# Kernel optimization log

Measured on AMD Instinct MI355X. Metric: run time of the kernel, lower is better.

Reference implementation:

```python
import jax, jax.numpy as jnp
import numpy as np

B, N, H = 4, 256, 128
T = 8  # triplet hidden width


def _linear_init(key, fan_in, fan_out):
    s = 1.0 / np.sqrt(fan_in)
    kw, kb = jax.random.split(key)
    W = jax.random.uniform(kw, (fan_in, fan_out), minval=-s, maxval=s, dtype=jnp.float32)
    b = jax.random.uniform(kb, (fan_out,), minval=-s, maxval=s, dtype=jnp.float32)
    return W, b


def setup_inputs() -> dict:
    key = jax.random.key(0)
    ks = jax.random.split(key, 16)
    inp = {
        "node_embeddings": jax.random.normal(ks[0], (B, N, H), dtype=jnp.float32),
        "edge_embeddings": jax.random.normal(ks[1], (B, N, H), dtype=jnp.float32),
        "graph_embeddings": jax.random.normal(ks[2], (B, H), dtype=jnp.float32),
        "previous_hidden": jax.random.normal(ks[3], (B, N, H), dtype=jnp.float32),
    }
    # message MLP: (z_i 2H, z_j 2H, edge_j H, graph H) = 6H -> H -> H -> H
    inp["Wm1"], inp["bm1"] = _linear_init(ks[4], 6 * H, H)
    inp["Wm2"], inp["bm2"] = _linear_init(ks[5], H, H)
    inp["Wm3"], inp["bm3"] = _linear_init(ks[6], H, H)
    # gate MLP: (z 2H, m H, edge H, graph H) = 5H -> H -> H (sigmoid)
    inp["Wg1"], inp["bg1"] = _linear_init(ks[7], 5 * H, H)
    inp["Wg2"], inp["bg2"] = _linear_init(ks[8], H, H)
    # readout: (z 2H, m H) = 3H -> H
    inp["Wr"], inp["br"] = _linear_init(ks[9], 3 * H, H)
    # triplet MLP: (node_j H, node_k H, node H, edge 3H, graph H) = 7H -> 8 (relu)
    inp["Wt1"], inp["bt1"] = _linear_init(ks[10], 7 * H, T)
    # triplet edge readout: 8 -> H
    inp["Wt2"], inp["bt2"] = _linear_init(ks[11], T, H)
    # layer norm params
    inp["gamma"] = jnp.ones((H,), dtype=jnp.float32)
    inp["beta"] = jnp.zeros((H,), dtype=jnp.float32)
    return inp


def reference(node_embeddings, edge_embeddings, graph_embeddings, previous_hidden,
              Wm1, bm1, Wm2, bm2, Wm3, bm3,
              Wg1, bg1, Wg2, bg2, Wr, br,
              Wt1, bt1, Wt2, bt2, gamma, beta):
    h = node_embeddings.shape[-1]
    z = jnp.concatenate([node_embeddings, previous_hidden], axis=-1)  # [B,N,2H]

    # ---- pairwise messages: decompose first linear so the 6H-wide concat is never built ----
    W_zi, W_zj = Wm1[: 2 * h], Wm1[2 * h: 4 * h]
    W_e, W_g = Wm1[4 * h: 5 * h], Wm1[5 * h:]
    u = z @ W_zi + (graph_embeddings @ W_g)[:, None, :] + bm1   # per-i part [B,N,H]
    v = z @ W_zj + edge_embeddings @ W_e                        # per-j part [B,N,H]
    h1 = jax.nn.relu(u[:, :, None, :] + v[:, None, :, :])       # [B,Ni,Nj,H]
    h2 = jax.nn.relu(h1 @ Wm2 + bm2)
    msgs = h2 @ Wm3 + bm3                                       # [B,Ni,Nj,H]
    m = jnp.max(msgs, axis=2)                                   # max over j -> [B,N,H]

    gb = jnp.broadcast_to(graph_embeddings[:, None, :], node_embeddings.shape)
    gate_in = jnp.concatenate([z, m, edge_embeddings, gb], axis=-1)  # [B,N,5H]
    g = jax.nn.sigmoid(jax.nn.relu(gate_in @ Wg1 + bg1) @ Wg2 + bg2)
    h_i = jnp.concatenate([z, m], axis=-1) @ Wr + br
    h_g = g * h_i + (1.0 - g) * previous_hidden

    # ---- triplet messages ----
    # pre-activation is separable over (j, k, i), so max over the N^2 (k,j) pairs
    # equals per-channel max_j + max_k (relu is monotone, max commutes with it).
    Wt_j, Wt_k, Wt_n = Wt1[:h], Wt1[h: 2 * h], Wt1[2 * h: 3 * h]
    Wt_e = Wt1[3 * h: 4 * h] + Wt1[4 * h: 5 * h] + Wt1[5 * h: 6 * h]
    Wt_g = Wt1[6 * h:]
    a_j = node_embeddings @ Wt_j   # [B,N,8]
    a_k = node_embeddings @ Wt_k   # [B,N,8]
    c = node_embeddings @ Wt_n + edge_embeddings @ Wt_e + (graph_embeddings @ Wt_g)[:, None, :] + bt1
    t_max = jax.nn.relu(c + jnp.max(a_j, axis=1, keepdims=True) + jnp.max(a_k, axis=1, keepdims=True))
    h_ij = t_max @ Wt2 + bt2       # [B,N,H]

    # ---- layer norm on gated hidden ----
    mu = jnp.mean(h_g, axis=-1, keepdims=True)
    var = jnp.mean(jnp.square(h_g - mu), axis=-1, keepdims=True)
    h_norm = (h_g - mu) * jax.lax.rsqrt(var + 1e-5) * gamma + beta
    return (h_norm, h_ij)
```

## Files before the change

### kernel.cpp

```cpp
#include <hip/hip_runtime.h>
#include <hip/hip_bf16.h>

typedef unsigned short u16;
typedef unsigned int u32;
typedef float f32x4 __attribute__((ext_vector_type(4)));
typedef short s16x8 __attribute__((ext_vector_type(8)));

#define MFMA16(a,b,c) __builtin_amdgcn_mfma_f32_16x16x32_bf16((a),(b),(c),0,0,0)

static __device__ __forceinline__ u16 f2bf(float x){
  union { __hip_bfloat16 b; u16 u; } c;
  c.b = __float2bfloat16(x);
  return c.u;
}

__global__ void prep_kernel(const float* __restrict__ Wm1, const float* __restrict__ Wm2,
                            const float* __restrict__ Wm3, const float* __restrict__ Wg1,
                            const float* __restrict__ Wr,  const float* __restrict__ Wt1,
                            const float* __restrict__ node,const float* __restrict__ prev,
                            const float* __restrict__ edge,const float* __restrict__ graph,
                            u16* __restrict__ WbT, u16* __restrict__ WgrT,
                            u16* __restrict__ Wm2T, u16* __restrict__ Wm3T,
                            u16* __restrict__ gin)
{
  int idx = blockIdx.x * 256 + threadIdx.x;
  if (idx < 147456) {
    int n = idx >> 9, k = idx & 511;
    int part = k >> 7, kk = k & 127;
    float v = 0.f;
    if (n < 128) {
      if (part == 0)      v = Wm1[kk*128 + n];
      else if (part == 1) v = Wm1[(128+kk)*128 + n];
      else if (part == 3) v = Wm1[(640+kk)*128 + n];
    } else if (n < 256) {
      int nn = n - 128;
      if (part == 0)      v = Wm1[(256+kk)*128 + nn];
      else if (part == 1) v = Wm1[(384+kk)*128 + nn];
      else if (part == 2) v = Wm1[(512+kk)*128 + nn];
    } else if (n < 280) {
      int tt = n - 256;
      if (tt < 8)       { if (part == 0) v = Wt1[kk*8 + tt]; }
      else if (tt < 16) { if (part == 0) v = Wt1[(128+kk)*8 + (tt-8)]; }
      else {
        int t = tt - 16;
        if (part == 0)      v = Wt1[(256+kk)*8 + t];
        else if (part == 2) v = Wt1[(384+kk)*8 + t] + Wt1[(512+kk)*8 + t] + Wt1[(640+kk)*8 + t];
        else if (part == 3) v = Wt1[(768+kk)*8 + t];
      }
    }
    WbT[idx] = f2bf(v);
    return;
  }
  idx -= 147456;
  if (idx < 163840) {
    int n = idx / 640, k = idx - n*640;
    int part = k >> 7, kk = k & 127;
    float v = 0.f;
    if (n < 128) {
      int r = (part==0) ? kk : (part==1) ? (128+kk) : (part==2) ? (384+kk)
                        : (part==3) ? (512+kk) : (256+kk);
      v = Wg1[r*128 + n];
    } else {
      int nn = n - 128;
      if (part == 0)      v = Wr[kk*128 + nn];
      else if (part == 1) v = Wr[(128+kk)*128 + nn];
      else if (part == 4) v = Wr[(256+kk)*128 + nn];
    }
    WgrT[idx] = f2bf(v);
    return;
  }
  idx -= 163840;
  if (idx < 16384) { int n = idx >> 7, k = idx & 127; Wm2T[idx] = f2bf(Wm2[k*128 + n]); return; }
  idx -= 16384;
  if (idx < 16384) { int n = idx >> 7, k = idx & 127; Wm3T[idx] = f2bf(Wm3[k*128 + n]); return; }
  idx -= 16384;
  {
    int row = idx >> 9, k = idx & 511;
    int part = k >> 7, kk = k & 127;
    float v;
    if (part == 0)      v = node[row*128 + kk];
    else if (part == 1) v = prev[row*128 + kk];
    else if (part == 2) v = edge[row*128 + kk];
    else                v = graph[(row >> 8)*128 + kk];
    gin[row*640 + k] = f2bf(v);
  }
}

__global__ void gemm_uvt_kernel(const u16* __restrict__ gin, const u16* __restrict__ WbT,
                                float* __restrict__ uvt)
{
  int m0 = blockIdx.x * 16, n0 = blockIdx.y * 16;
  int lane = threadIdx.x;
  int lrow = lane & 15, lgrp = lane >> 4;
  const u16* arow = gin + (size_t)(m0 + lrow) * 640;
  const u16* brow = WbT + (size_t)(n0 + lrow) * 512;
  f32x4 acc = {0.f, 0.f, 0.f, 0.f};
#pragma unroll
  for (int k0 = 0; k0 < 16; ++k0) {
    s16x8 a = *reinterpret_cast<const s16x8*>(arow + k0*32 + lgrp*8);
    s16x8 b = *reinterpret_cast<const s16x8*>(brow + k0*32 + lgrp*8);
    acc = MFMA16(a, b, acc);
  }
#pragma unroll
  for (int r = 0; r < 4; ++r)
    uvt[(size_t)(m0 + lgrp*4 + r) * 288 + n0 + lrow] = acc[r];
}

__global__ void maxat_kernel(const float* __restrict__ uvt, float* __restrict__ mjk)
{
  int b = blockIdx.x;
  int tid = threadIdx.x;
  int row = b*256 + tid;
  __shared__ float part[4][16];
  float v[16];
#pragma unroll
  for (int t = 0; t < 16; ++t) v[t] = uvt[(size_t)row*288 + 256 + t];
#pragma unroll
  for (int off = 32; off >= 1; off >>= 1) {
#pragma unroll
    for (int t = 0; t < 16; ++t) v[t] = fmaxf(v[t], __shfl_xor(v[t], off));
  }
  int wid = tid >> 6;
  if ((tid & 63) == 0) {
#pragma unroll
    for (int t = 0; t < 16; ++t) part[wid][t] = v[t];
  }
  __syncthreads();
  if (tid < 16)
    mjk[b*16 + tid] = fmaxf(fmaxf(part[0][tid], part[1][tid]),
                            fmaxf(part[2][tid], part[3][tid]));
}

__global__ __launch_bounds__(256) void msgmax_kernel(const float* __restrict__ uvt,
    const u16* __restrict__ Wm2T, const u16* __restrict__ Wm3T,
    const float* __restrict__ bm1, const float* __restrict__ bm2,
    const float* __restrict__ bm3, u16* __restrict__ gin)
{
  const int row = blockIdx.x;
  const int b   = row >> 8;
  const int tid = threadIdx.x;
  const int w   = tid >> 6;
  const int lane = tid & 63;
  const int c = lane & 15, g = lane >> 4;

  __shared__ u16 a1s[2][4][16][32];
  __shared__ u16 h2s[2][16][136];

  s16x8 wb2[4][2], wb3[4][2];
#pragma unroll
  for (int mt = 0; mt < 2; ++mt) {
    int col = w*32 + mt*16 + c;
#pragma unroll
    for (int k0 = 0; k0 < 4; ++k0) {
      wb2[k0][mt] = *reinterpret_cast<const s16x8*>(Wm2T + col*128 + k0*32 + g*8);
      wb3[k0][mt] = *reinterpret_cast<const s16x8*>(Wm3T + col*128 + k0*32 + g*8);
    }
  }
  float4 bm2v[2];
#pragma unroll
  for (int mt = 0; mt < 2; ++mt)
    bm2v[mt] = *reinterpret_cast<const float4*>(bm2 + w*32 + mt*16 + 4*g);

  const float* urow = uvt + (size_t)row * 288;
  float uf[8];
  {
    int off = w*32 + g*8;
    float4 x = *reinterpret_cast<const float4*>(urow + off);
    float4 y = *reinterpret_cast<const float4*>(urow + off + 4);
    float4 p = *reinterpret_cast<const float4*>(bm1 + off);
    float4 q = *reinterpret_cast<const float4*>(bm1 + off + 4);
    uf[0]=x.x+p.x; uf[1]=x.y+p.y; uf[2]=x.z+p.z; uf[3]=x.w+p.w;
    uf[4]=y.x+q.x; uf[5]=y.y+q.y; uf[6]=y.z+q.z; uf[7]=y.w+q.w;
  }

  const float* vb = uvt + (size_t)(b*256) * 288 + 128;
  f32x4 mmax[2];
#pragma unroll
  for (int mt = 0; mt < 2; ++mt)
#pragma unroll
    for (int r = 0; r < 4; ++r) mmax[mt][r] = -1e30f;

  float4 vc[2][2];
#define LOADV(IT) do { \
  _Pragma("unroll") \
  for (int t = 0; t < 2; ++t) { \
    const float* p_ = vb + (size_t)((IT)*32 + t*16 + c) * 288 + w*32 + g*8; \
    vc[t][0] = *reinterpret_cast<const float4*>(p_); \
    vc[t][1] = *reinterpret_cast<const float4*>(p_ + 4); } } while (0)

  LOADV(0);

  for (int it = 0; it < 8; ++it) {
#pragma unroll
    for (int t = 0; t < 2; ++t) {
      u32 d0 = (u32)f2bf(fmaxf(uf[0] + vc[t][0].x, 0.f))
             | ((u32)f2bf(fmaxf(uf[1] + vc[t][0].y, 0.f)) << 16);
      u32 d1 = (u32)f2bf(fmaxf(uf[2] + vc[t][0].z, 0.f))
             | ((u32)f2bf(fmaxf(uf[3] + vc[t][0].w, 0.f)) << 16);
      u32 d2 = (u32)f2bf(fmaxf(uf[4] + vc[t][1].x, 0.f))
             | ((u32)f2bf(fmaxf(uf[5] + vc[t][1].y, 0.f)) << 16);
      u32 d3 = (u32)f2bf(fmaxf(uf[6] + vc[t][1].z, 0.f))
             | ((u32)f2bf(fmaxf(uf[7] + vc[t][1].w, 0.f)) << 16);
      uint4 pk = {d0, d1, d2, d3};
      *reinterpret_cast<uint4*>(&a1s[t][w][c][g*8]) = pk;
    }
    if (it < 7) LOADV(it + 1);
    __syncthreads();

    f32x4 acc1[2][2] = {{{0,0,0,0},{0,0,0,0}},{{0,0,0,0},{0,0,0,0}}};
#pragma unroll
    for (int t = 0; t < 2; ++t)
#pragma unroll
      for (int k0 = 0; k0 < 4; ++k0) {
        s16x8 af = *reinterpret_cast<const s16x8*>(&a1s[t][k0][c][g*8]);
        acc1[t][0] = MFMA16(wb2[k0][0], af, acc1[t][0]);
        acc1[t][1] = MFMA16(wb2[k0][1], af, acc1[t][1]);
      }

#pragma unroll
    for (int t = 0; t < 2; ++t)
#pragma unroll
      for (int mt = 0; mt < 2; ++mt) {
        u32 lo = (u32)f2bf(fmaxf(acc1[t][mt][0] + bm2v[mt].x, 0.f))
               | ((u32)f2bf(fmaxf(acc1[t][mt][1] + bm2v[mt].y, 0.f)) << 16);
        u32 hi = (u32)f2bf(fmaxf(acc1[t][mt][2] + bm2v[mt].z, 0.f))
               | ((u32)f2bf(fmaxf(acc1[t][mt][3] + bm2v[mt].w, 0.f)) << 16);
        uint2 pk = {lo, hi};
        *reinterpret_cast<uint2*>(&h2s[t][c][w*32 + mt*16 + 4*g]) = pk;
      }
    __syncthreads();

    f32x4 acc2[2][2] = {{{0,0,0,0},{0,0,0,0}},{{0,0,0,0},{0,0,0,0}}};
#pragma unroll
    for (int t = 0; t < 2; ++t)
#pragma unroll
      for (int k0 = 0; k0 < 4; ++k0) {
        s16x8 a2 = *reinterpret_cast<const s16x8*>(&h2s[t][c][k0*32 + g*8]);
        acc2[t][0] = MFMA16(wb3[k0][0], a2, acc2[t][0]);
        acc2[t][1] = MFMA16(wb3[k0][1], a2, acc2[t][1]);
      }
#pragma unroll
    for (int mt = 0; mt < 2; ++mt)
#pragma unroll
      for (int r = 0; r < 4; ++r)
        mmax[mt][r] = fmaxf(mmax[mt][r], fmaxf(acc2[0][mt][r], acc2[1][mt][r]));
  }
#undef LOADV

#pragma unroll
  for (int mt = 0; mt < 2; ++mt) {
    f32x4 m = mmax[mt];
#pragma unroll
    for (int off = 1; off < 16; off <<= 1) {
      m[0] = fmaxf(m[0], __shfl_xor(m[0], off));
      m[1] = fmaxf(m[1], __shfl_xor(m[1], off));
      m[2] = fmaxf(m[2], __shfl_xor(m[2], off));
      m[3] = fmaxf(m[3], __shfl_xor(m[3], off));
    }
    if (c == 0) {
      int col = w*32 + mt*16 + 4*g;
      u32 lo = (u32)f2bf(m[0] + bm3[col])   | ((u32)f2bf(m[1] + bm3[col+1]) << 16);
      u32 hi = (u32)f2bf(m[2] + bm3[col+2]) | ((u32)f2bf(m[3] + bm3[col+3]) << 16);
      uint2 pk = {lo, hi};
      *reinterpret_cast<uint2*>(gin + (size_t)row*640 + 512 + col) = pk;
    }
  }
}

__global__ void gemm_gate_kernel(const u16* __restrict__ gin, const u16* __restrict__ WgrT,
                                 const float* __restrict__ bg1, const float* __restrict__ br,
                                 float* __restrict__ r1, float* __restrict__ hi)
{
  int m0 = blockIdx.x * 16, n0 = blockIdx.y * 16;
  int lane = threadIdx.x;
  int lrow = lane & 15, lgrp = lane >> 4;
  const u16* arow = gin  + (size_t)(m0 + lrow) * 640;
  const u16* brow = WgrT + (size_t)(n0 + lrow) * 640;
  f32x4 acc = {0.f, 0.f, 0.f, 0.f};
#pragma unroll
  for (int k0 = 0; k0 < 20; ++k0) {
    s16x8 a = *reinterpret_cast<const s16x8*>(arow + k0*32 + lgrp*8);
    s16x8 b = *reinterpret_cast<const s16x8*>(brow + k0*32 + lgrp*8);
    acc = MFMA16(a, b, acc);
  }
  int col = n0 + lrow;
  float bv = (col < 128) ? bg1[col] : br[col - 128];
#pragma unroll
  for (int r = 0; r < 4; ++r) {
    int gr = m0 + lgrp*4 + r;
    if (col < 128) r1[gr*128 + col] = fmaxf(acc[r] + bv, 0.f);
    else           hi[gr*128 + col - 128] = acc[r] + bv;
  }
}

__global__ void finalize_kernel(const float* __restrict__ r1, const float* __restrict__ hi,
                                const float* __restrict__ prev, const float* __restrict__ uvt,
                                const float* __restrict__ mjk,
                                const float* __restrict__ Wg2, const float* __restrict__ bg2,
                                const float* __restrict__ bt1, const float* __restrict__ Wt2,
                                const float* __restrict__ bt2, const float* __restrict__ gamma,
                                const float* __restrict__ beta, float* __restrict__ out)
{
  int row = blockIdx.x;
  int h = threadIdx.x;
  int b = row >> 8;
  __shared__ float r1s[128];
  __shared__ float red[4];
  r1s[h] = r1[row*128 + h];
  __syncthreads();
  float glin = bg2[h];
#pragma unroll 8
  for (int k = 0; k < 128; ++k) glin += r1s[k] * Wg2[k*128 + h];
  float g = 1.f / (1.f + __expf(-glin));
  float hg = g * hi[row*128 + h] + (1.f - g) * prev[row*128 + h];

  float s1 = hg, s2 = hg*hg;
#pragma unroll
  for (int off = 1; off < 64; off <<= 1) {
    s1 += __shfl_xor(s1, off);
    s2 += __shfl_xor(s2, off);
  }
  int wid = h >> 6;
  if ((h & 63) == 0) { red[wid] = s1; red[2 + wid] = s2; }
  __syncthreads();
  float mu  = (red[0] + red[1]) * 0.0078125f;
  float ex2 = (red[2] + red[3]) * 0.0078125f;
  float var = ex2 - mu*mu;
  float hn = (hg - mu) * rsqrtf(var + 1e-5f) * gamma[h] + beta[h];
  out[row*128 + h] = hn;

  float o2 = bt2[h];
#pragma unroll
  for (int t = 0; t < 8; ++t) {
    float tv = uvt[(size_t)row*288 + 272 + t] + bt1[t] + mjk[b*16 + t] + mjk[b*16 + 8 + t];
    tv = fmaxf(tv, 0.f);
    o2 += tv * Wt2[t*128 + h];
  }
  out[131072 + row*128 + h] = o2;
}

extern "C" void kernel_launch(void* const* d_in, const int* in_sizes, int n_in,
                              void* d_out, int out_size, void* d_ws, size_t ws_size,
                              hipStream_t stream) {
  const float* node  = (const float*)d_in[0];
  const float* edge  = (const float*)d_in[1];
  const float* graph = (const float*)d_in[2];
  const float* prev  = (const float*)d_in[3];
  const float* Wm1 = (const float*)d_in[4];
  const float* bm1 = (const float*)d_in[5];
  const float* Wm2 = (const float*)d_in[6];
  const float* bm2 = (const float*)d_in[7];
  const float* Wm3 = (const float*)d_in[8];
  const float* bm3 = (const float*)d_in[9];
  const float* Wg1 = (const float*)d_in[10];
  const float* bg1 = (const float*)d_in[11];
  const float* Wg2 = (const float*)d_in[12];
  const float* bg2 = (const float*)d_in[13];
  const float* Wr  = (const float*)d_in[14];
  const float* br  = (const float*)d_in[15];
  const float* Wt1 = (const float*)d_in[16];
  const float* bt1 = (const float*)d_in[17];
  const float* Wt2 = (const float*)d_in[18];
  const float* bt2 = (const float*)d_in[19];
  const float* gamma = (const float*)d_in[20];
  const float* beta  = (const float*)d_in[21];
  float* out = (float*)d_out;

  char* ws = (char*)d_ws;
  u16*   WbT  = (u16*)(ws + 0);
  u16*   WgrT = (u16*)(ws + 294912);
  u16*   Wm2T = (u16*)(ws + 622592);
  u16*   Wm3T = (u16*)(ws + 655360);
  u16*   gin  = (u16*)(ws + 688128);
  float* uvt  = (float*)(ws + 1998848);
  float* r1   = (float*)(ws + 3178496);
  float* hi   = (float*)(ws + 3702784);
  float* mjk  = (float*)(ws + 4227072);

  prep_kernel<<<3392, 256, 0, stream>>>(Wm1, Wm2, Wm3, Wg1, Wr, Wt1,
                                        node, prev, edge, graph,
                                        WbT, WgrT, Wm2T, Wm3T, gin);
  gemm_uvt_kernel<<<dim3(64, 18), 64, 0, stream>>>(gin, WbT, uvt);
  maxat_kernel<<<4, 256, 0, stream>>>(uvt, mjk);
  msgmax_kernel<<<1024, 256, 0, stream>>>(uvt, Wm2T, Wm3T, bm1, bm2, bm3, gin);
  gemm_gate_kernel<<<dim3(64, 16), 64, 0, stream>>>(gin, WgrT, bg1, br, r1, hi);
  finalize_kernel<<<1024, 128, 0, stream>>>(r1, hi, prev, uvt, mjk,
                                            Wg2, bg2, bt1, Wt2, bt2, gamma, beta, out);
}
```

Before: 61.21 us.

## Software-pipeline msgmax GEMM stages with double-buffered LDS and fewer barriers

Restructures the msgmax inner loop so that GEMM2 of the current tile and GEMM1 of the next tile share one barrier interval, with a1s and h2s double-buffered and global loads prefetched two iterations ahead. This halves the __syncthreads per iteration and lets MFMA work of adjacent stages interleave. It also pads the a1s rows from 32 to 40 elements to reduce LDS bank conflicts, and adds a min-blocks hint of 4 to the launch bounds. The cost is more LDS, more live registers for the deeper prefetch, and occupancy pressure from the launch-bounds hint.

```diff
diff --git a/kernel.cpp b/kernel.cpp
--- a/kernel.cpp
+++ b/kernel.cpp
@@ -131,7 +131,7 @@
                             fmaxf(part[2][tid], part[3][tid]));
 }
 
-__global__ __launch_bounds__(256) void msgmax_kernel(const float* __restrict__ uvt,
+__global__ __launch_bounds__(256, 4) void msgmax_kernel(const float* __restrict__ uvt,
     const u16* __restrict__ Wm2T, const u16* __restrict__ Wm3T,
     const float* __restrict__ bm1, const float* __restrict__ bm2,
     const float* __restrict__ bm3, u16* __restrict__ gin)
@@ -143,8 +143,8 @@
   const int lane = tid & 63;
   const int c = lane & 15, g = lane >> 4;
 
-  __shared__ u16 a1s[2][4][16][32];
-  __shared__ u16 h2s[2][16][136];
+  __shared__ u16 a1s[2][2][4][16][40];
+  __shared__ u16 h2s[2][2][16][136];
 
   s16x8 wb2[4][2], wb3[4][2];
 #pragma unroll
@@ -188,64 +188,77 @@
     vc[t][0] = *reinterpret_cast<const float4*>(p_); \
     vc[t][1] = *reinterpret_cast<const float4*>(p_ + 4); } } while (0)
 
+#define A1W(BUF) do { \
+  _Pragma("unroll") \
+  for (int t = 0; t < 2; ++t) { \
+    u32 d0 = (u32)f2bf(fmaxf(uf[0] + vc[t][0].x, 0.f)) \
+           | ((u32)f2bf(fmaxf(uf[1] + vc[t][0].y, 0.f)) << 16); \
+    u32 d1 = (u32)f2bf(fmaxf(uf[2] + vc[t][0].z, 0.f)) \
+           | ((u32)f2bf(fmaxf(uf[3] + vc[t][0].w, 0.f)) << 16); \
+    u32 d2 = (u32)f2bf(fmaxf(uf[4] + vc[t][1].x, 0.f)) \
+           | ((u32)f2bf(fmaxf(uf[5] + vc[t][1].y, 0.f)) << 16); \
+    u32 d3 = (u32)f2bf(fmaxf(uf[6] + vc[t][1].z, 0.f)) \
+           | ((u32)f2bf(fmaxf(uf[7] + vc[t][1].w, 0.f)) << 16); \
+    uint4 pk = {d0, d1, d2, d3}; \
+    *reinterpret_cast<uint4*>(&a1s[BUF][t][w][c][g*8]) = pk; } } while (0)
+
+#define GEMM1(AB, HB) do { \
+  f32x4 acc1[2][2] = {{{0,0,0,0},{0,0,0,0}},{{0,0,0,0},{0,0,0,0}}}; \
+  _Pragma("unroll") \
+  for (int t = 0; t < 2; ++t) \
+    _Pragma("unroll") \
+    for (int k0 = 0; k0 < 4; ++k0) { \
+      s16x8 af = *reinterpret_cast<const s16x8*>(&a1s[AB][t][k0][c][g*8]); \
+      acc1[t][0] = MFMA16(wb2[k0][0], af, acc1[t][0]); \
+      acc1[t][1] = MFMA16(wb2[k0][1], af, acc1[t][1]); \
+    } \
+  _Pragma("unroll") \
+  for (int t = 0; t < 2; ++t) \
+    _Pragma("unroll") \
+    for (int mt = 0; mt < 2; ++mt) { \
+      u32 lo = (u32)f2bf(fmaxf(acc1[t][mt][0] + bm2v[mt].x, 0.f)) \
+             | ((u32)f2bf(fmaxf(acc1[t][mt][1] + bm2v[mt].y, 0.f)) << 16); \
+      u32 hi = (u32)f2bf(fmaxf(acc1[t][mt][2] + bm2v[mt].z, 0.f)) \
+             | ((u32)f2bf(fmaxf(acc1[t][mt][3] + bm2v[mt].w, 0.f)) << 16); \
+      uint2 pk = {lo, hi}; \
+      *reinterpret_cast<uint2*>(&h2s[HB][t][c][w*32 + mt*16 + 4*g]) = pk; } } while (0)
+
+#define GEMM2(HB) do { \
+  f32x4 acc2[2][2] = {{{0,0,0,0},{0,0,0,0}},{{0,0,0,0},{0,0,0,0}}}; \
+  _Pragma("unroll") \
+  for (int t = 0; t < 2; ++t) \
+    _Pragma("unroll") \
+    for (int k0 = 0; k0 < 4; ++k0) { \
+      s16x8 a2 = *reinterpret_cast<const s16x8*>(&h2s[HB][t][c][k0*32 + g*8]); \
+      acc2[t][0] = MFMA16(wb3[k0][0], a2, acc2[t][0]); \
+      acc2[t][1] = MFMA16(wb3[k0][1], a2, acc2[t][1]); \
+    } \
+  _Pragma("unroll") \
+  for (int mt = 0; mt < 2; ++mt) \
+    _Pragma("unroll") \
+    for (int r = 0; r < 4; ++r) \
+      mmax[mt][r] = fmaxf(mmax[mt][r], fmaxf(acc2[0][mt][r], acc2[1][mt][r])); } while (0)
+
   LOADV(0);
+  A1W(0);
+  LOADV(1);
+  __syncthreads();
+  GEMM1(0, 0);
 
   for (int it = 0; it < 8; ++it) {
-#pragma unroll
-    for (int t = 0; t < 2; ++t) {
-      u32 d0 = (u32)f2bf(fmaxf(uf[0] + vc[t][0].x, 0.f))
-             | ((u32)f2bf(fmaxf(uf[1] + vc[t][0].y, 0.f)) << 16);
-      u32 d1 = (u32)f2bf(fmaxf(uf[2] + vc[t][0].z, 0.f))
-             | ((u32)f2bf(fmaxf(uf[3] + vc[t][0].w, 0.f)) << 16);
-      u32 d2 = (u32)f2bf(fmaxf(uf[4] + vc[t][1].x, 0.f))
-             | ((u32)f2bf(fmaxf(uf[5] + vc[t][1].y, 0.f)) << 16);
-      u32 d3 = (u32)f2bf(fmaxf(uf[6] + vc[t][1].z, 0.f))
-             | ((u32)f2bf(fmaxf(uf[7] + vc[t][1].w, 0.f)) << 16);
-      uint4 pk = {d0, d1, d2, d3};
-      *reinterpret_cast<uint4*>(&a1s[t][w][c][g*8]) = pk;
-    }
-    if (it < 7) LOADV(it + 1);
+    int nb = (it + 1) & 1;
+    if (it < 7) {
+      A1W(nb);
+      if (it < 6) LOADV(it + 2);
+    }
     __syncthreads();
-
-    f32x4 acc1[2][2] = {{{0,0,0,0},{0,0,0,0}},{{0,0,0,0},{0,0,0,0}}};
-#pragma unroll
-    for (int t = 0; t < 2; ++t)
-#pragma unroll
-      for (int k0 = 0; k0 < 4; ++k0) {
-        s16x8 af = *reinterpret_cast<const s16x8*>(&a1s[t][k0][c][g*8]);
-        acc1[t][0] = MFMA16(wb2[k0][0], af, acc1[t][0]);
-        acc1[t][1] = MFMA16(wb2[k0][1], af, acc1[t][1]);
-      }
-
-#pragma unroll
-    for (int t = 0; t < 2; ++t)
-#pragma unroll
-      for (int mt = 0; mt < 2; ++mt) {
-        u32 lo = (u32)f2bf(fmaxf(acc1[t][mt][0] + bm2v[mt].x, 0.f))
-               | ((u32)f2bf(fmaxf(acc1[t][mt][1] + bm2v[mt].y, 0.f)) << 16);
-        u32 hi = (u32)f2bf(fmaxf(acc1[t][mt][2] + bm2v[mt].z, 0.f))
-               | ((u32)f2bf(fmaxf(acc1[t][mt][3] + bm2v[mt].w, 0.f)) << 16);
-        uint2 pk = {lo, hi};
-        *reinterpret_cast<uint2*>(&h2s[t][c][w*32 + mt*16 + 4*g]) = pk;
-      }
-    __syncthreads();
-
-    f32x4 acc2[2][2] = {{{0,0,0,0},{0,0,0,0}},{{0,0,0,0},{0,0,0,0}}};
-#pragma unroll
-    for (int t = 0; t < 2; ++t)
-#pragma unroll
-      for (int k0 = 0; k0 < 4; ++k0) {
-        s16x8 a2 = *reinterpret_cast<const s16x8*>(&h2s[t][c][k0*32 + g*8]);
-        acc2[t][0] = MFMA16(wb3[k0][0], a2, acc2[t][0]);
-        acc2[t][1] = MFMA16(wb3[k0][1], a2, acc2[t][1]);
-      }
-#pragma unroll
-    for (int mt = 0; mt < 2; ++mt)
-#pragma unroll
-      for (int r = 0; r < 4; ++r)
-        mmax[mt][r] = fmaxf(mmax[mt][r], fmaxf(acc2[0][mt][r], acc2[1][mt][r]));
+    GEMM2(it & 1);
+    if (it < 7) GEMM1(nb, nb);
   }
 #undef LOADV
+#undef A1W
+#undef GEMM1
+#undef GEMM2
 
 #pragma unroll
   for (int mt = 0; mt < 2; ++mt) {
```

Result: slower. 75.70 us (+23.7%).

## Restructure msgmax to 2 waves with per-wave 64 columns and register A-operand

Applied to the files above, without the earlier changes.

The pairwise message kernel now runs 128 threads (2 waves) per row, each wave owning 64 output columns. The first-layer activations are built directly in registers as MFMA operands, which removes the a1s shared buffer and one barrier per iteration. The j loop walks 16-row tiles with a double-buffered h2s, so each iteration needs a single sync. Register pressure roughly doubles (32 weight fragments per lane), and the prefetch of the next V tile is dropped, which could cut occupancy or expose load latency.

```diff
diff --git a/kernel.cpp b/kernel.cpp
--- a/kernel.cpp
+++ b/kernel.cpp
@@ -131,7 +131,7 @@
                             fmaxf(part[2][tid], part[3][tid]));
 }
 
-__global__ __launch_bounds__(256) void msgmax_kernel(const float* __restrict__ uvt,
+__global__ __launch_bounds__(128) void msgmax_kernel(const float* __restrict__ uvt,
     const u16* __restrict__ Wm2T, const u16* __restrict__ Wm3T,
     const float* __restrict__ bm1, const float* __restrict__ bm2,
     const float* __restrict__ bm3, u16* __restrict__ gin)
@@ -143,112 +143,93 @@
   const int lane = tid & 63;
   const int c = lane & 15, g = lane >> 4;
 
-  __shared__ u16 a1s[2][4][16][32];
-  __shared__ u16 h2s[2][16][136];
-
-  s16x8 wb2[4][2], wb3[4][2];
-#pragma unroll
-  for (int mt = 0; mt < 2; ++mt) {
-    int col = w*32 + mt*16 + c;
+  __shared__ u16 h2s[2][4][16][40];
+
+  s16x8 wb2[4][4], wb3[4][4];
+#pragma unroll
+  for (int mt = 0; mt < 4; ++mt) {
+    int col = w*64 + mt*16 + c;
 #pragma unroll
     for (int k0 = 0; k0 < 4; ++k0) {
       wb2[k0][mt] = *reinterpret_cast<const s16x8*>(Wm2T + col*128 + k0*32 + g*8);
       wb3[k0][mt] = *reinterpret_cast<const s16x8*>(Wm3T + col*128 + k0*32 + g*8);
     }
   }
-  float4 bm2v[2];
-#pragma unroll
-  for (int mt = 0; mt < 2; ++mt)
-    bm2v[mt] = *reinterpret_cast<const float4*>(bm2 + w*32 + mt*16 + 4*g);
-
-  const float* urow = uvt + (size_t)row * 288;
-  float uf[8];
+  f32x4 bm2v[4];
+#pragma unroll
+  for (int mt = 0; mt < 4; ++mt)
+    bm2v[mt] = *reinterpret_cast<const f32x4*>(bm2 + w*64 + mt*16 + 4*g);
+
+  f32x4 uf[4][2];
   {
-    int off = w*32 + g*8;
-    float4 x = *reinterpret_cast<const float4*>(urow + off);
-    float4 y = *reinterpret_cast<const float4*>(urow + off + 4);
-    float4 p = *reinterpret_cast<const float4*>(bm1 + off);
-    float4 q = *reinterpret_cast<const float4*>(bm1 + off + 4);
-    uf[0]=x.x+p.x; uf[1]=x.y+p.y; uf[2]=x.z+p.z; uf[3]=x.w+p.w;
-    uf[4]=y.x+q.x; uf[5]=y.y+q.y; uf[6]=y.z+q.z; uf[7]=y.w+q.w;
+    const float* urow = uvt + (size_t)row * 288;
+#pragma unroll
+    for (int k0 = 0; k0 < 4; ++k0) {
+      int off = k0*32 + g*8;
+      uf[k0][0] = *reinterpret_cast<const f32x4*>(urow + off)
+                + *reinterpret_cast<const f32x4*>(bm1 + off);
+      uf[k0][1] = *reinterpret_cast<const f32x4*>(urow + off + 4)
+                + *reinterpret_cast<const f32x4*>(bm1 + off + 4);
+    }
   }
 
   const float* vb = uvt + (size_t)(b*256) * 288 + 128;
-  f32x4 mmax[2];
-#pragma unroll
-  for (int mt = 0; mt < 2; ++mt)
-#pragma unroll
-    for (int r = 0; r < 4; ++r) mmax[mt][r] = -1e30f;
-
-  float4 vc[2][2];
-#define LOADV(IT) do { \
-  _Pragma("unroll") \
-  for (int t = 0; t < 2; ++t) { \
-    const float* p_ = vb + (size_t)((IT)*32 + t*16 + c) * 288 + w*32 + g*8; \
-    vc[t][0] = *reinterpret_cast<const float4*>(p_); \
-    vc[t][1] = *reinterpret_cast<const float4*>(p_ + 4); } } while (0)
-
-  LOADV(0);
-
-  for (int it = 0; it < 8; ++it) {
-#pragma unroll
-    for (int t = 0; t < 2; ++t) {
-      u32 d0 = (u32)f2bf(fmaxf(uf[0] + vc[t][0].x, 0.f))
-             | ((u32)f2bf(fmaxf(uf[1] + vc[t][0].y, 0.f)) << 16);
-      u32 d1 = (u32)f2bf(fmaxf(uf[2] + vc[t][0].z, 0.f))
-             | ((u32)f2bf(fmaxf(uf[3] + vc[t][0].w, 0.f)) << 16);
-      u32 d2 = (u32)f2bf(fmaxf(uf[4] + vc[t][1].x, 0.f))
-             | ((u32)f2bf(fmaxf(uf[5] + vc[t][1].y, 0.f)) << 16);
-      u32 d3 = (u32)f2bf(fmaxf(uf[6] + vc[t][1].z, 0.f))
-             | ((u32)f2bf(fmaxf(uf[7] + vc[t][1].w, 0.f)) << 16);
-      uint4 pk = {d0, d1, d2, d3};
-      *reinterpret_cast<uint4*>(&a1s[t][w][c][g*8]) = pk;
-    }
-    if (it < 7) LOADV(it + 1);
+  const f32x4 z4 = {0.f, 0.f, 0.f, 0.f};
+  f32x4 mmax[4];
+#pragma unroll
+  for (int mt = 0; mt < 4; ++mt) mmax[mt] = {-1e30f, -1e30f, -1e30f, -1e30f};
+
+  for (int jt = 0; jt < 16; ++jt) {
+    const float* vrow = vb + (size_t)(jt*16 + c) * 288 + g*8;
+    s16x8 a1f[4];
+#pragma unroll
+    for (int k0 = 0; k0 < 4; ++k0) {
+      f32x4 lo = __builtin_elementwise_max(
+                   *reinterpret_cast<const f32x4*>(vrow + k0*32) + uf[k0][0], z4);
+      f32x4 hi = __builtin_elementwise_max(
+                   *reinterpret_cast<const f32x4*>(vrow + k0*32 + 4) + uf[k0][1], z4);
+      s16x8 f;
+      f[0] = (short)f2bf(lo[0]); f[1] = (short)f2bf(lo[1]);
+      f[2] = (short)f2bf(lo[2]); f[3] = (short)f2bf(lo[3]);
+      f[4] = (short)f2bf(hi[0]); f[5] = (short)f2bf(hi[1]);
+      f[6] = (short)f2bf(hi[2]); f[7] = (short)f2bf(hi[3]);
+      a1f[k0] = f;
+    }
+
+    f32x4 acc1[4] = {z4, z4, z4, z4};
+#pragma unroll
+    for (int k0 = 0; k0 < 4; ++k0) {
+#pragma unroll
+      for (int mt = 0; mt < 4; ++mt)
+        acc1[mt] = MFMA16(wb2[k0][mt], a1f[k0], acc1[mt]);
+    }
+
+    int buf = jt & 1;
+#pragma unroll
+    for (int mt = 0; mt < 4; ++mt) {
+      f32x4 t = __builtin_elementwise_max(acc1[mt] + bm2v[mt], z4);
+      u32 lo = (u32)f2bf(t[0]) | ((u32)f2bf(t[1]) << 16);
+      u32 hi = (u32)f2bf(t[2]) | ((u32)f2bf(t[3]) << 16);
+      uint2 pk = {lo, hi};
+      *reinterpret_cast<uint2*>(&h2s[buf][w*2 + (mt>>1)][c][(mt&1)*16 + 4*g]) = pk;
+    }
     __syncthreads();
 
-    f32x4 acc1[2][2] = {{{0,0,0,0},{0,0,0,0}},{{0,0,0,0},{0,0,0,0}}};
-#pragma unroll
-    for (int t = 0; t < 2; ++t)
-#pragma unroll
-      for (int k0 = 0; k0 < 4; ++k0) {
-        s16x8 af = *reinterpret_cast<const s16x8*>(&a1s[t][k0][c][g*8]);
-        acc1[t][0] = MFMA16(wb2[k0][0], af, acc1[t][0]);
-        acc1[t][1] = MFMA16(wb2[k0][1], af, acc1[t][1]);
-      }
-
-#pragma unroll
-    for (int t = 0; t < 2; ++t)
-#pragma unroll
-      for (int mt = 0; mt < 2; ++mt) {
-        u32 lo = (u32)f2bf(fmaxf(acc1[t][mt][0] + bm2v[mt].x, 0.f))
-               | ((u32)f2bf(fmaxf(acc1[t][mt][1] + bm2v[mt].y, 0.f)) << 16);
-        u32 hi = (u32)f2bf(fmaxf(acc1[t][mt][2] + bm2v[mt].z, 0.f))
-               | ((u32)f2bf(fmaxf(acc1[t][mt][3] + bm2v[mt].w, 0.f)) << 16);
-        uint2 pk = {lo, hi};
-        *reinterpret_cast<uint2*>(&h2s[t][c][w*32 + mt*16 + 4*g]) = pk;
-      }
-    __syncthreads();
-
-    f32x4 acc2[2][2] = {{{0,0,0,0},{0,0,0,0}},{{0,0,0,0},{0,0,0,0}}};
-#pragma unroll
-    for (int t = 0; t < 2; ++t)
-#pragma unroll
-      for (int k0 = 0; k0 < 4; ++k0) {
-        s16x8 a2 = *reinterpret_cast<const s16x8*>(&h2s[t][c][k0*32 + g*8]);
-        acc2[t][0] = MFMA16(wb3[k0][0], a2, acc2[t][0]);
-        acc2[t][1] = MFMA16(wb3[k0][1], a2, acc2[t][1]);
-      }
-#pragma unroll
-    for (int mt = 0; mt < 2; ++mt)
-#pragma unroll
-      for (int r = 0; r < 4; ++r)
-        mmax[mt][r] = fmaxf(mmax[mt][r], fmaxf(acc2[0][mt][r], acc2[1][mt][r]));
-  }
-#undef LOADV
-
-#pragma unroll
-  for (int mt = 0; mt < 2; ++mt) {
+    f32x4 acc2[4] = {z4, z4, z4, z4};
+#pragma unroll
+    for (int k0 = 0; k0 < 4; ++k0) {
+      s16x8 a2 = *reinterpret_cast<const s16x8*>(&h2s[buf][k0][c][g*8]);
+#pragma unroll
+      for (int mt = 0; mt < 4; ++mt)
+        acc2[mt] = MFMA16(wb3[k0][mt], a2, acc2[mt]);
+    }
+#pragma unroll
+    for (int mt = 0; mt < 4; ++mt)
+      mmax[mt] = __builtin_elementwise_max(mmax[mt], acc2[mt]);
+  }
+
+#pragma unroll
+  for (int mt = 0; mt < 4; ++mt) {
     f32x4 m = mmax[mt];
 #pragma unroll
     for (int off = 1; off < 16; off <<= 1) {
@@ -258,7 +239,7 @@
       m[3] = fmaxf(m[3], __shfl_xor(m[3], off));
     }
     if (c == 0) {
-      int col = w*32 + mt*16 + 4*g;
+      int col = w*64 + mt*16 + 4*g;
       u32 lo = (u32)f2bf(m[0] + bm3[col])   | ((u32)f2bf(m[1] + bm3[col+1]) << 16);
       u32 hi = (u32)f2bf(m[2] + bm3[col+2]) | ((u32)f2bf(m[3] + bm3[col+3]) << 16);
       uint2 pk = {lo, hi};
@@ -382,7 +363,7 @@
                                         WbT, WgrT, Wm2T, Wm3T, gin);
   gemm_uvt_kernel<<<dim3(64, 18), 64, 0, stream>>>(gin, WbT, uvt);
   maxat_kernel<<<4, 256, 0, stream>>>(uvt, mjk);
-  msgmax_kernel<<<1024, 256, 0, stream>>>(uvt, Wm2T, Wm3T, bm1, bm2, bm3, gin);
+  msgmax_kernel<<<1024, 128, 0, stream>>>(uvt, Wm2T, Wm3T, bm1, bm2, bm3, gin);
   gemm_gate_kernel<<<dim3(64, 16), 64, 0, stream>>>(gin, WgrT, bg1, br, r1, hi);
   finalize_kernel<<<1024, 128, 0, stream>>>(r1, hi, prev, uvt, mjk,
                                             Wg2, bg2, bt1, Wt2, bt2, gamma, beta, out);
```

Measured after the change: 71.98 us. 1.18x slower.
